# Kernel optimization log

Measured on AMD Instinct MI355X. Metric: run time of the kernel, lower is better.

Reference implementation:

```python
import jax, jax.numpy as jnp
import numpy as np

N = 50000      # nodes
E = 800000     # edges (before self loops)
D = 256        # in_features
SMALL = 25     # floor(D/10)


def setup_inputs() -> dict:
    key = jax.random.key(0)
    k1, k2, k3, k4, k5 = jax.random.split(key, 5)
    x = jax.random.normal(k1, (N, D), jnp.float32)
    src = jax.random.randint(k2, (E,), 0, N)
    dst = jax.random.randint(k3, (E,), 0, N)
    Wq = jax.random.normal(k4, (D, SMALL), jnp.float32) / np.float32(np.sqrt(D))
    bq = jnp.zeros((SMALL,), jnp.float32)
    Wk = jax.random.normal(k5, (D, SMALL), jnp.float32) / np.float32(np.sqrt(D))
    bk = jnp.zeros((SMALL,), jnp.float32)
    return {"x": x, "src": src, "dst": dst, "Wq": Wq, "bq": bq, "Wk": Wk, "bk": bk}


def reference(x, src, dst, Wq, bq, Wk, bk):
    d_k = np.float32(np.sqrt(SMALL))  # self.d_k = sqrt(small_in_features)
    q = jnp.tanh(x @ Wq + bq)         # query head: Linear + Tanh, [N, SMALL]
    k = x @ Wk + bk                   # key head: Linear,          [N, SMALL]
    # dgl.add_self_loop: append (i, i) for every node
    loop = jnp.arange(N, dtype=src.dtype)
    s = jnp.concatenate([src, loop])  # [E+N]
    d = jnp.concatenate([dst, loop])  # [E+N]
    # edge weight = <query[src], key[dst]> / d_k
    w = jnp.sum(q[s] * k[d], axis=1) / d_k            # [E+N]
    # segment softmax over incoming edges of each destination node
    wmax = jax.ops.segment_max(w, d, num_segments=N)  # every node has a self loop -> no empty segments
    ew = jnp.exp(w - wmax[d])
    denom = jax.ops.segment_sum(ew, d, num_segments=N)
    alpha = ew / denom[d]                             # [E+N]
    # weighted scatter-sum of src node features
    out = jax.ops.segment_sum(alpha[:, None] * x[s], d, num_segments=N)  # [N, D]
    return out
```

## Files before the change

### kernel.cpp

```cpp
#include <hip/hip_runtime.h>
#include <math.h>

#define D 256
#define SM 25
#define QS 32
#define WROWS 264
#define NCH 4
#define NT 8

typedef short bf16x8 __attribute__((ext_vector_type(8)));
typedef float f32x4  __attribute__((ext_vector_type(4)));

__device__ __forceinline__ unsigned int bf16rne(float f) {
    unsigned int u = __float_as_uint(f);
    return (u + 0x7fffu + ((u >> 16) & 1u)) >> 16;
}
__device__ __forceinline__ float bl(unsigned int lo16) {
    return __uint_as_float(lo16 << 16);
}
__device__ __forceinline__ float bh(unsigned int u) {
    return __uint_as_float(u & 0xffff0000u);
}

__global__ __launch_bounds__(256) void prep_kernel(
    const float* __restrict__ Wq, const float* __restrict__ bq,
    const float* __restrict__ Wk, const float* __restrict__ bk,
    unsigned short* __restrict__ wt_g,
    float* __restrict__ bias_g,
    int* __restrict__ cnt, int N) {
    int gid = blockIdx.x * 256 + threadIdx.x;
    if (gid < N) cnt[gid] = 0;
    if (gid < 64 * 256) {
        int j = gid >> 8, k = gid & 255;
        float w = 0.f;
        if (j < SM) w = Wq[k * SM + j];
        else if (j < 2 * SM) w = Wk[k * SM + (j - SM)];
        wt_g[j * 256 + k] = (unsigned short)bf16rne(w);
    }
    if (gid >= 16384 && gid < 16448) {
        int t = gid - 16384;
        bias_g[t] = (t < SM) ? bq[t] : ((t < 2 * SM) ? bk[t - SM] : 0.f);
    }
}

__global__ __launch_bounds__(256) void qk_kernel(
    const float* __restrict__ x,
    const unsigned short* __restrict__ wt_g, const float* __restrict__ bias_g,
    const int4* __restrict__ dst4, const int* __restrict__ dste,
    unsigned short* __restrict__ xt,
    float* __restrict__ qp,
    float* __restrict__ kp,
    int* __restrict__ cnt, int N, int E) {
    __shared__ __align__(16) short xs[64 * WROWS];
    __shared__ float bias[64];
    int t = threadIdx.x;
    int n0 = blockIdx.x * 64;

    {
        int r = t >> 2, qtr = t & 3;
        int row = n0 + r; if (row >= N) row = N - 1;
        const float4* xr = (const float4*)(x + (size_t)row * D) + qtr * 16;
        short* dst = xs + r * WROWS + qtr * 64;
#pragma unroll
        for (int i = 0; i < 16; ++i) {
            float4 a = xr[i];
            unsigned int w0 = bf16rne(a.x) | (bf16rne(a.y) << 16);
            unsigned int w1 = bf16rne(a.z) | (bf16rne(a.w) << 16);
            *(uint2*)(dst + i * 4) = make_uint2(w0, w1);
        }
    }
    if (t < 64) bias[t] = bias_g[t];
    __syncthreads();

    for (int o = 0; o < 8; ++o) {
        int idx = o * 256 + t;
        int r = idx >> 5, c = idx & 31;
        int row = n0 + r;
        if (row < N) {
            uint4 v = *(const uint4*)(xs + r * WROWS + c * 8);
            int tile = c >> 2;
            ((uint4*)xt)[((size_t)tile * N + row) * 4 + (c & 3)] = v;
        }
    }

    int wid = t >> 6, lane = t & 63;
    int mm = lane & 15, g = lane >> 4;
    f32x4 acc[4];
#pragma unroll
    for (int tt = 0; tt < 4; ++tt) acc[tt] = (f32x4){0.f, 0.f, 0.f, 0.f};
    const short* arow = xs + (wid * 16 + mm) * WROWS + g * 8;
#pragma unroll
    for (int ks = 0; ks < 8; ++ks) {
        bf16x8 af = *(const bf16x8*)(arow + ks * 32);
#pragma unroll
        for (int tt = 0; tt < 4; ++tt) {
            bf16x8 bf = *(const bf16x8*)((const short*)wt_g +
                                         (tt * 16 + mm) * 256 + g * 8 + ks * 32);
            acc[tt] = __builtin_amdgcn_mfma_f32_16x16x32_bf16(af, bf, acc[tt], 0, 0, 0);
        }
    }
#pragma unroll
    for (int tt = 0; tt < 4; ++tt) {
        int j = tt * 16 + mm;
#pragma unroll
        for (int r = 0; r < 4; ++r) {
            int node = n0 + wid * 16 + g * 4 + r;
            if (node >= N) continue;
            float v = acc[tt][r] + bias[j];
            if (j < SM)           qp[(size_t)node * QS + j] = tanhf(v);
            else if (j < 2 * SM)  kp[(size_t)node * QS + (j - SM)] = v;
            else if (j < 57)      qp[(size_t)node * QS + (j - SM)] = 0.f;
            else                  kp[(size_t)node * QS + (j - 32)] = 0.f;
        }
    }

    int gid = blockIdx.x * 256 + t;
    int n4e = E >> 2;
    if (gid < n4e) {
        int4 dd = dst4[gid];
        atomicAdd(&cnt[dd.x], 1);
        atomicAdd(&cnt[dd.y], 1);
        atomicAdd(&cnt[dd.z], 1);
        atomicAdd(&cnt[dd.w], 1);
    }
    if (gid == 0) {
        for (int e = n4e * 4; e < E; ++e) atomicAdd(&cnt[dste[e]], 1);
    }
}

__global__ __launch_bounds__(256) void scan_a_kernel(const int4* __restrict__ cnt4,
                                                     int* __restrict__ bsum, int n4) {
    __shared__ int wsum[4];
    int t = threadIdx.x;
    int idx = blockIdx.x * 256 + t;
    int s = 0;
    if (idx < n4) { int4 v = cnt4[idx]; s = v.x + v.y + v.z + v.w; }
#pragma unroll
    for (int o = 32; o; o >>= 1) s += __shfl_xor(s, o);
    if ((t & 63) == 0) wsum[t >> 6] = s;
    __syncthreads();
    if (t == 0) bsum[blockIdx.x] = wsum[0] + wsum[1] + wsum[2] + wsum[3];
}

__global__ __launch_bounds__(256) void scan_c_kernel(const int4* __restrict__ cnt4,
                                                     const int* __restrict__ bsum,
                                                     int* __restrict__ offN,
                                                     int4* __restrict__ off4,
                                                     int4* __restrict__ cursor4,
                                                     int n4, int nblk) {
    __shared__ int wsum[4];
    int t = threadIdx.x;
    int lane = t & 63;
    int bv = (lane < nblk) ? bsum[lane] : 0;
    int bincl = bv;
#pragma unroll
    for (int o = 1; o < 64; o <<= 1) {
        int u = __shfl_up(bincl, o);
        if (lane >= o) bincl += u;
    }
    int blockbase = __shfl(bincl - bv, blockIdx.x);
    int total = __shfl(bincl, nblk - 1);
    if (blockIdx.x == 0 && t == 0) *offN = total;
    int idx = blockIdx.x * 256 + t;
    int4 v = make_int4(0, 0, 0, 0);
    if (idx < n4) v = cnt4[idx];
    int s0 = v.x, s01 = s0 + v.y, s012 = s01 + v.z, s = s012 + v.w;
    int incl = s;
#pragma unroll
    for (int o = 1; o < 64; o <<= 1) {
        int u = __shfl_up(incl, o);
        if (lane >= o) incl += u;
    }
    if (lane == 63) wsum[t >> 6] = incl;
    __syncthreads();
    int w = t >> 6;
    int wbase = 0;
    for (int i = 0; i < w; ++i) wbase += wsum[i];
    int base = blockbase + wbase + (incl - s);
    if (idx < n4) {
        int4 o4 = make_int4(base, base + s0, base + s01, base + s012);
        off4[idx]    = o4;
        cursor4[idx] = o4;
    }
}

__global__ void scatter_kernel(const int4* __restrict__ src4, const int4* __restrict__ dst4,
                               const int* __restrict__ srce, const int* __restrict__ dste,
                               int* __restrict__ cursor, int* __restrict__ csr_src,
                               int n4e, int E) {
    int e = blockIdx.x * blockDim.x + threadIdx.x;
    if (e >= n4e) return;
    int4 s = src4[e];
    int4 d = dst4[e];
    csr_src[atomicAdd(&cursor[d.x], 1)] = s.x;
    csr_src[atomicAdd(&cursor[d.y], 1)] = s.y;
    csr_src[atomicAdd(&cursor[d.z], 1)] = s.z;
    csr_src[atomicAdd(&cursor[d.w], 1)] = s.w;
    if (e == 0) {
        for (int i = n4e * 4; i < E; ++i)
            csr_src[atomicAdd(&cursor[dste[i]], 1)] = srce[i];
    }
}

__global__ __launch_bounds__(256) void score_kernel(
        const float* __restrict__ qp, const float* __restrict__ kp,
        const int* __restrict__ off, const int* __restrict__ csr_src,
        float* __restrict__ alphaS, float* __restrict__ alphaE, int N) {
    int lane = threadIdx.x & 63;
    int v = blockIdx.x * 4 + (threadIdx.x >> 6);
    if (v >= N) return;
    int lo = off[v];
    int deg1 = off[v + 1] - lo + 1;
    const float4* kd4 = (const float4*)(kp + (size_t)v * QS);
    float4 kd[7];
#pragma unroll
    for (int j = 0; j < 7; ++j) kd[j] = kd4[j];

    float wv[NCH];
    float m = -INFINITY;
#pragma unroll
    for (int c = 0; c < NCH; ++c) {
        int i = c * 64 + lane;
        float wcur = -INFINITY;
        if (c * 64 < deg1 && i < deg1) {
            int s = v;
            if (i > 0) s = csr_src[lo + i - 1];
            const float4* q4 = (const float4*)(qp + (size_t)s * QS);
            float acc = 0.f;
#pragma unroll
            for (int j = 0; j < 7; ++j) {
                float4 a = q4[j];
                acc += a.x*kd[j].x + a.y*kd[j].y + a.z*kd[j].z + a.w*kd[j].w;
            }
            wcur = acc * 0.2f;
        }
        wv[c] = wcur;
        m = fmaxf(m, wcur);
    }
#pragma unroll
    for (int o = 32; o; o >>= 1) m = fmaxf(m, __shfl_xor(m, o));
    float ssum = 0.f;
#pragma unroll
    for (int c = 0; c < NCH; ++c) {
        float e = (wv[c] == -INFINITY) ? 0.f : __expf(wv[c] - m);
        wv[c] = e;
        ssum += e;
    }
#pragma unroll
    for (int o = 32; o; o >>= 1) ssum += __shfl_xor(ssum, o);
    float inv = 1.f / ssum;

#pragma unroll
    for (int c = 0; c < NCH; ++c) {
        int i = c * 64 + lane;
        if (c * 64 < deg1 && i < deg1) {
            float a = wv[c] * inv;
            if (i == 0) alphaS[v] = a;
            else        alphaE[lo + i - 1] = a;
        }
    }
}

__global__ __launch_bounds__(256) void gather_kernel(
        const unsigned int* __restrict__ xt,
        const float* __restrict__ alphaS, const float* __restrict__ alphaE,
        const int* __restrict__ off, const int* __restrict__ csr_src,
        float* __restrict__ out, int N) {
    int tile = blockIdx.x & (NT - 1);
    int nb = blockIdx.x >> 3;
    int t = threadIdx.x;
    int g = t >> 4;
    int l = t & 15;
    int v = nb * 16 + g;
    if (v >= N) return;
    const unsigned int* xbase = xt + (size_t)tile * N * 16 + l;
    int lo = off[v], hi = off[v + 1];
    float ax = 0.f, ay = 0.f;
    {
        float a = alphaS[v];
        unsigned int u = xbase[(size_t)v * 16];
        ax += a * bl(u); ay += a * bh(u);
    }
    int e = lo;
    for (; e + 4 <= hi; e += 4) {
        float a0 = alphaE[e];     int s0 = csr_src[e];
        float a1 = alphaE[e + 1]; int s1 = csr_src[e + 1];
        float a2 = alphaE[e + 2]; int s2 = csr_src[e + 2];
        float a3 = alphaE[e + 3]; int s3 = csr_src[e + 3];
        unsigned int u0 = xbase[(size_t)s0 * 16];
        unsigned int u1 = xbase[(size_t)s1 * 16];
        unsigned int u2 = xbase[(size_t)s2 * 16];
        unsigned int u3 = xbase[(size_t)s3 * 16];
        ax += a0 * bl(u0); ay += a0 * bh(u0);
        ax += a1 * bl(u1); ay += a1 * bh(u1);
        ax += a2 * bl(u2); ay += a2 * bh(u2);
        ax += a3 * bl(u3); ay += a3 * bh(u3);
    }
    for (; e < hi; ++e) {
        float a = alphaE[e];
        int   s = csr_src[e];
        unsigned int u = xbase[(size_t)s * 16];
        ax += a * bl(u); ay += a * bh(u);
    }
    *(float2*)(out + (size_t)v * D + tile * 32 + l * 2) = make_float2(ax, ay);
}

extern "C" void kernel_launch(void* const* d_in, const int* in_sizes, int n_in,
                              void* d_out, int out_size, void* d_ws, size_t ws_size,
                              hipStream_t stream) {
    const float* x   = (const float*)d_in[0];
    const int*   src = (const int*)d_in[1];
    const int*   dst = (const int*)d_in[2];
    const float* Wq  = (const float*)d_in[3];
    const float* bq  = (const float*)d_in[4];
    const float* Wk  = (const float*)d_in[5];
    const float* bk  = (const float*)d_in[6];
    float* out = (float*)d_out;

    int N = in_sizes[0] / D;
    int E = in_sizes[1];

    char* p = (char*)d_ws;
    auto alloc = [&](size_t bytes) {
        char* r = p;
        p += (bytes + 255) & ~(size_t)255;
        return r;
    };
    unsigned short* xt   = (unsigned short*)alloc((size_t)N * D * sizeof(unsigned short));
    unsigned short* wt_g = (unsigned short*)alloc(64 * 256 * sizeof(unsigned short));
    float* bias_g  = (float*)alloc(64 * sizeof(float));
    float* qp      = (float*)alloc((size_t)N * QS * sizeof(float));
    float* kp      = (float*)alloc((size_t)N * QS * sizeof(float));
    int*   cnt     = (int*)  alloc((size_t)(N + 4) * sizeof(int));
    int*   off     = (int*)  alloc((size_t)(N + 4) * sizeof(int));
    int*   cursor  = (int*)  alloc((size_t)(N + 4) * sizeof(int));
    int*   csr_src = (int*)  alloc((size_t)E * sizeof(int));
    int*   bsum    = (int*)  alloc(64 * sizeof(int));
    float* alphaS  = (float*)alloc((size_t)N * sizeof(float));
    float* alphaE  = (float*)alloc((size_t)E * sizeof(float));

    int prepgrid = (N > 16448 ? N : 16448);
    prep_kernel<<<(prepgrid + 255) / 256, 256, 0, stream>>>(
        Wq, bq, Wk, bk, wt_g, bias_g, cnt, N);
    int nqk = (N + 63) / 64;
    qk_kernel<<<nqk, 256, 0, stream>>>(x, wt_g, bias_g, (const int4*)dst, dst,
                                       xt, qp, kp, cnt, N, E);
    int n4 = (N + 3) / 4;
    int nblk = (n4 + 255) / 256;
    scan_a_kernel<<<nblk, 256, 0, stream>>>((const int4*)cnt, bsum, n4);
    scan_c_kernel<<<nblk, 256, 0, stream>>>((const int4*)cnt, bsum, off + N,
                                            (int4*)off, (int4*)cursor, n4, nblk);
    int n4e = E / 4;
    scatter_kernel<<<(n4e + 255) / 256, 256, 0, stream>>>(
        (const int4*)src, (const int4*)dst, src, dst, cursor, csr_src, n4e, E);
    score_kernel<<<(N + 3) / 4, 256, 0, stream>>>(qp, kp, off, csr_src,
                                                  alphaS, alphaE, N);
    int ngb = (N + 15) / 16;
    gather_kernel<<<ngb * NT, 256, 0, stream>>>((const unsigned int*)xt,
                                                alphaS, alphaE, off, csr_src,
                                                out, N);
}
```

Before: 325.8 us.

## Interleave edge source and alpha into int2 CSR with self-loop slot; split gather per node

The CSR now reserves a slot per node for the self loop and stores source index and softmax weight together as an int2, so score writes alpha in place and gather reads one 8-byte record per edge instead of two separate arrays. The gather kernel now assigns one wavefront per node, with four 16-lane subgroups striding over edges and a shuffle reduction at the end, instead of 16 lanes per node. This is meant to improve memory-level parallelism for high-degree nodes and cut separate index and alpha loads. In exchange it launches four times as many gather blocks, adds cross-lane reductions, and scatter now does partial 4-byte stores into 8-byte records.

Result: slower. 389.6 us (+19.6%).

```diff
diff --git a/kernel.cpp b/kernel.cpp
--- a/kernel.cpp
+++ b/kernel.cpp
@@ -147,7 +147,7 @@
                                                      int* __restrict__ offN,
                                                      int4* __restrict__ off4,
                                                      int4* __restrict__ cursor4,
-                                                     int n4, int nblk) {
+                                                     int n4, int nblk, int N) {
     __shared__ int wsum[4];
     int t = threadIdx.x;
     int lane = t & 63;
@@ -160,7 +160,7 @@
     }
     int blockbase = __shfl(bincl - bv, blockIdx.x);
     int total = __shfl(bincl, nblk - 1);
-    if (blockIdx.x == 0 && t == 0) *offN = total;
+    if (blockIdx.x == 0 && t == 0) *offN = total + N;
     int idx = blockIdx.x * 256 + t;
     int4 v = make_int4(0, 0, 0, 0);
     if (idx < n4) v = cnt4[idx];
@@ -178,39 +178,42 @@
     for (int i = 0; i < w; ++i) wbase += wsum[i];
     int base = blockbase + wbase + (incl - s);
     if (idx < n4) {
-        int4 o4 = make_int4(base, base + s0, base + s01, base + s012);
+        int node0 = idx * 4;
+        int4 o4 = make_int4(base + node0,
+                            base + s0   + node0 + 1,
+                            base + s01  + node0 + 2,
+                            base + s012 + node0 + 3);
         off4[idx]    = o4;
-        cursor4[idx] = o4;
+        cursor4[idx] = make_int4(o4.x + 1, o4.y + 1, o4.z + 1, o4.w + 1);
     }
 }
 
 __global__ void scatter_kernel(const int4* __restrict__ src4, const int4* __restrict__ dst4,
                                const int* __restrict__ srce, const int* __restrict__ dste,
-                               int* __restrict__ cursor, int* __restrict__ csr_src,
+                               int* __restrict__ cursor, int2* __restrict__ ea2,
                                int n4e, int E) {
     int e = blockIdx.x * blockDim.x + threadIdx.x;
     if (e >= n4e) return;
     int4 s = src4[e];
     int4 d = dst4[e];
-    csr_src[atomicAdd(&cursor[d.x], 1)] = s.x;
-    csr_src[atomicAdd(&cursor[d.y], 1)] = s.y;
-    csr_src[atomicAdd(&cursor[d.z], 1)] = s.z;
-    csr_src[atomicAdd(&cursor[d.w], 1)] = s.w;
+    ea2[atomicAdd(&cursor[d.x], 1)].x = s.x;
+    ea2[atomicAdd(&cursor[d.y], 1)].x = s.y;
+    ea2[atomicAdd(&cursor[d.z], 1)].x = s.z;
+    ea2[atomicAdd(&cursor[d.w], 1)].x = s.w;
     if (e == 0) {
         for (int i = n4e * 4; i < E; ++i)
-            csr_src[atomicAdd(&cursor[dste[i]], 1)] = srce[i];
+            ea2[atomicAdd(&cursor[dste[i]], 1)].x = srce[i];
     }
 }
 
 __global__ __launch_bounds__(256) void score_kernel(
         const float* __restrict__ qp, const float* __restrict__ kp,
-        const int* __restrict__ off, const int* __restrict__ csr_src,
-        float* __restrict__ alphaS, float* __restrict__ alphaE, int N) {
+        const int* __restrict__ off2, int2* __restrict__ ea2, int N) {
     int lane = threadIdx.x & 63;
     int v = blockIdx.x * 4 + (threadIdx.x >> 6);
     if (v >= N) return;
-    int lo = off[v];
-    int deg1 = off[v + 1] - lo + 1;
+    int lo2 = off2[v];
+    int deg1 = off2[v + 1] - lo2;
     const float4* kd4 = (const float4*)(kp + (size_t)v * QS);
     float4 kd[7];
 #pragma unroll
@@ -223,8 +226,7 @@
         int i = c * 64 + lane;
         float wcur = -INFINITY;
         if (c * 64 < deg1 && i < deg1) {
-            int s = v;
-            if (i > 0) s = csr_src[lo + i - 1];
+            int s = (i == 0) ? v : ea2[lo2 + i].x;
             const float4* q4 = (const float4*)(qp + (size_t)s * QS);
             float acc = 0.f;
 #pragma unroll
@@ -254,55 +256,50 @@
     for (int c = 0; c < NCH; ++c) {
         int i = c * 64 + lane;
         if (c * 64 < deg1 && i < deg1) {
-            float a = wv[c] * inv;
-            if (i == 0) alphaS[v] = a;
-            else        alphaE[lo + i - 1] = a;
+            int ab = __float_as_int(wv[c] * inv);
+            if (i == 0) ea2[lo2] = make_int2(v, ab);
+            else        ea2[lo2 + i].y = ab;
         }
     }
 }
 
 __global__ __launch_bounds__(256) void gather_kernel(
         const unsigned int* __restrict__ xt,
-        const float* __restrict__ alphaS, const float* __restrict__ alphaE,
-        const int* __restrict__ off, const int* __restrict__ csr_src,
+        const int2* __restrict__ ea2, const int* __restrict__ off2,
         float* __restrict__ out, int N) {
     int tile = blockIdx.x & (NT - 1);
     int nb = blockIdx.x >> 3;
-    int t = threadIdx.x;
-    int g = t >> 4;
-    int l = t & 15;
-    int v = nb * 16 + g;
+    int w = threadIdx.x >> 6;
+    int lane = threadIdx.x & 63;
+    int sub = lane >> 4;
+    int col = lane & 15;
+    int v = nb * 4 + w;
     if (v >= N) return;
-    const unsigned int* xbase = xt + (size_t)tile * N * 16 + l;
-    int lo = off[v], hi = off[v + 1];
+    int lo = off2[v];
+    int deg1 = off2[v + 1] - lo;
+    const unsigned int* xb = xt + (size_t)tile * N * 16 + col;
     float ax = 0.f, ay = 0.f;
-    {
-        float a = alphaS[v];
-        unsigned int u = xbase[(size_t)v * 16];
-        ax += a * bl(u); ay += a * bh(u);
-    }
-    int e = lo;
-    for (; e + 4 <= hi; e += 4) {
-        float a0 = alphaE[e];     int s0 = csr_src[e];
-        float a1 = alphaE[e + 1]; int s1 = csr_src[e + 1];
-        float a2 = alphaE[e + 2]; int s2 = csr_src[e + 2];
-        float a3 = alphaE[e + 3]; int s3 = csr_src[e + 3];
-        unsigned int u0 = xbase[(size_t)s0 * 16];
-        unsigned int u1 = xbase[(size_t)s1 * 16];
-        unsigned int u2 = xbase[(size_t)s2 * 16];
-        unsigned int u3 = xbase[(size_t)s3 * 16];
+    int i = sub;
+    for (; i + 4 < deg1; i += 8) {
+        int2 r0 = ea2[lo + i];
+        int2 r1 = ea2[lo + i + 4];
+        float a0 = __int_as_float(r0.y);
+        float a1 = __int_as_float(r1.y);
+        unsigned int u0 = xb[(size_t)r0.x * 16];
+        unsigned int u1 = xb[(size_t)r1.x * 16];
         ax += a0 * bl(u0); ay += a0 * bh(u0);
         ax += a1 * bl(u1); ay += a1 * bh(u1);
-        ax += a2 * bl(u2); ay += a2 * bh(u2);
-        ax += a3 * bl(u3); ay += a3 * bh(u3);
-    }
-    for (; e < hi; ++e) {
-        float a = alphaE[e];
-        int   s = csr_src[e];
-        unsigned int u = xbase[(size_t)s * 16];
-        ax += a * bl(u); ay += a * bh(u);
-    }
-    *(float2*)(out + (size_t)v * D + tile * 32 + l * 2) = make_float2(ax, ay);
+    }
+    if (i < deg1) {
+        int2 r0 = ea2[lo + i];
+        float a0 = __int_as_float(r0.y);
+        unsigned int u0 = xb[(size_t)r0.x * 16];
+        ax += a0 * bl(u0); ay += a0 * bh(u0);
+    }
+    ax += __shfl_xor(ax, 16); ay += __shfl_xor(ay, 16);
+    ax += __shfl_xor(ax, 32); ay += __shfl_xor(ay, 32);
+    if (sub == 0)
+        *(float2*)(out + (size_t)v * D + tile * 32 + col * 2) = make_float2(ax, ay);
 }
 
 extern "C" void kernel_launch(void* const* d_in, const int* in_sizes, int n_in,
@@ -334,10 +331,8 @@
     int*   cnt     = (int*)  alloc((size_t)(N + 4) * sizeof(int));
     int*   off     = (int*)  alloc((size_t)(N + 4) * sizeof(int));
     int*   cursor  = (int*)  alloc((size_t)(N + 4) * sizeof(int));
-    int*   csr_src = (int*)  alloc((size_t)E * sizeof(int));
+    int2*  ea2     = (int2*) alloc((size_t)(N + E + 4) * sizeof(int2));
     int*   bsum    = (int*)  alloc(64 * sizeof(int));
-    float* alphaS  = (float*)alloc((size_t)N * sizeof(float));
-    float* alphaE  = (float*)alloc((size_t)E * sizeof(float));
 
     int prepgrid = (N > 16448 ? N : 16448);
     prep_kernel<<<(prepgrid + 255) / 256, 256, 0, stream>>>(
@@ -349,14 +344,12 @@
     int nblk = (n4 + 255) / 256;
     scan_a_kernel<<<nblk, 256, 0, stream>>>((const int4*)cnt, bsum, n4);
     scan_c_kernel<<<nblk, 256, 0, stream>>>((const int4*)cnt, bsum, off + N,
-                                            (int4*)off, (int4*)cursor, n4, nblk);
+                                            (int4*)off, (int4*)cursor, n4, nblk, N);
     int n4e = E / 4;
     scatter_kernel<<<(n4e + 255) / 256, 256, 0, stream>>>(
-        (const int4*)src, (const int4*)dst, src, dst, cursor, csr_src, n4e, E);
-    score_kernel<<<(N + 3) / 4, 256, 0, stream>>>(qp, kp, off, csr_src,
-                                                  alphaS, alphaE, N);
-    int ngb = (N + 15) / 16;
+        (const int4*)src, (const int4*)dst, src, dst, cursor, ea2, n4e, E);
+    score_kernel<<<(N + 3) / 4, 256, 0, stream>>>(qp, kp, off, ea2, N);
+    int ngb = (N + 3) / 4;
     gather_kernel<<<ngb * NT, 256, 0, stream>>>((const unsigned int*)xt,
-                                                alphaS, alphaE, off, csr_src,
-                                                out, N);
-}
+                                                (const int2*)ea2, off, out, N);
+}
```
